# Performance work log

Measured on AMD Instinct MI355X. Metric: run time of the kernel, lower is better.

The kernel has to match this reference:

```python
import jax, jax.numpy as jnp
import numpy as np

NU = 200000  # num users
NI = 200000  # num items
H = 64
L = 2
E = 4000000
P = 100000
EPS = 1e-5


def _seg_mean(msgs, dst, n):
    # msgs: [E, H] gathered source features, dst: [E] destination ids
    s = jax.ops.segment_sum(msgs, dst, num_segments=n)
    c = jax.ops.segment_sum(jnp.ones((msgs.shape[0],), msgs.dtype), dst, num_segments=n)
    return s / jnp.maximum(c, 1.0)[:, None]


def _bn(x, g, b, m, v):
    return (x - m) * jax.lax.rsqrt(v + EPS) * g + b


def setup_inputs() -> dict:
    key = jax.random.key(0)
    ks = jax.random.split(key, 12)
    s = 1.0 / np.sqrt(H)
    inp = {
        "edge_index": jax.random.randint(ks[0], (2, E), 0, NU),
        "edge_label_index": jax.random.randint(ks[1], (2, P), 0, NU),
        "user_emb": jax.random.normal(ks[2], (NU, H), jnp.float32) * 0.1,
        "item_emb": jax.random.normal(ks[3], (NI, H), jnp.float32) * 0.1,
        "u_ll_w": jax.random.normal(ks[4], (L, H, H), jnp.float32) * s,
        "u_ll_b": jnp.zeros((L, H), jnp.float32),
        "u_lr_w": jax.random.normal(ks[5], (L, H, H), jnp.float32) * s,
        "i_ll_w": jax.random.normal(ks[6], (L, H, H), jnp.float32) * s,
        "i_ll_b": jnp.zeros((L, H), jnp.float32),
        "i_lr_w": jax.random.normal(ks[7], (L, H, H), jnp.float32) * s,
        "u_bn_g": jnp.ones((L, H), jnp.float32),
        "u_bn_b": jnp.zeros((L, H), jnp.float32),
        "u_bn_m": jnp.zeros((L, H), jnp.float32),
        "u_bn_v": jnp.ones((L, H), jnp.float32),
        "i_bn_g": jnp.ones((L, H), jnp.float32),
        "i_bn_b": jnp.zeros((L, H), jnp.float32),
        "i_bn_m": jnp.zeros((L, H), jnp.float32),
        "i_bn_v": jnp.ones((L, H), jnp.float32),
        "fc1_w": jax.random.normal(ks[8], (2 * H, H), jnp.float32) * (1.0 / np.sqrt(2 * H)),
        "fc1_b": jnp.zeros((H,), jnp.float32),
        "fc2_w": jax.random.normal(ks[9], (H, 4), jnp.float32) * s,
        "fc2_b": jnp.zeros((4,), jnp.float32),
    }
    return inp


def reference(edge_index, edge_label_index, user_emb, item_emb,
              u_ll_w, u_ll_b, u_lr_w, i_ll_w, i_ll_b, i_lr_w,
              u_bn_g, u_bn_b, u_bn_m, u_bn_v,
              i_bn_g, i_bn_b, i_bn_m, i_bn_v,
              fc1_w, fc1_b, fc2_w, fc2_b):
    src, dst = edge_index[0], edge_index[1]  # user -> item edges
    user_x, item_x = user_emb, item_emb
    for l in range(L):
        # user update: aggregate item features along flipped edges (item->user)
        agg_u = _seg_mean(item_x[dst], src, NU)          # [NU, H]
        u_new = agg_u @ u_ll_w[l] + u_ll_b[l] + user_x @ u_lr_w[l]
        u_new = jax.nn.relu(_bn(u_new, u_bn_g[l], u_bn_b[l], u_bn_m[l], u_bn_v[l]))
        # item update: aggregate (old) user features along user->item edges
        agg_i = _seg_mean(user_x[src], dst, NI)          # [NI, H]
        i_new = agg_i @ i_ll_w[l] + i_ll_b[l] + item_x @ i_lr_w[l]
        i_new = jax.nn.relu(_bn(i_new, i_bn_g[l], i_bn_b[l], i_bn_m[l], i_bn_v[l]))
        user_x, item_x = u_new, i_new
    u_h = user_x[edge_label_index[0]]                    # [P, H]
    i_h = item_x[edge_label_index[1]]                    # [P, H]
    x = jnp.concatenate([u_h, i_h], axis=1)              # [P, 2H]
    x = jax.nn.relu(x @ fc1_w + fc1_b)
    return x @ fc2_w + fc2_b                             # [P, 4]
```

## Files before the change

### kernel.cpp

```cpp
#include <hip/hip_runtime.h>

#define NU 200000
#define NI 200000
#define NN 400000
#define H 64
#define NE 4000000
#define NP 100000
#define EPSF 1e-5f

#define BSH 9
#define BNODES 512
#define NB ((NN + BNODES - 1) / BNODES)
#define CAP 15104

#define PBLOCKS 512
#define EPB 7816

#define DUMMY 200000
#define NROW 200002

typedef unsigned short u16;
typedef __attribute__((ext_vector_type(8))) short bf16x8;
typedef __attribute__((ext_vector_type(4))) float f32x4;

__device__ __forceinline__ u16 f2bf(float f) {
    unsigned int b = __float_as_uint(f);
    b += 0x7FFFu + ((b >> 16) & 1u);
    return (u16)(b >> 16);
}


__global__ __launch_bounds__(256) void part1_kernel(
    const int* __restrict__ src, const int* __restrict__ dst,
    int* __restrict__ blkhist)
{
    __shared__ int hist[NB];
    int tid = threadIdx.x, blk = blockIdx.x;
    for (int i = tid; i < NB; i += 256) hist[i] = 0;
    __syncthreads();
    int e0 = blk * EPB, e1 = min(NE, e0 + EPB);
    for (int e = e0 + tid * 4; e + 4 <= e1; e += 1024) {
        int4 s4 = *(const int4*)&src[e];
        int4 d4 = *(const int4*)&dst[e];
        atomicAdd(&hist[s4.x >> BSH], 1); atomicAdd(&hist[(NU + d4.x) >> BSH], 1);
        atomicAdd(&hist[s4.y >> BSH], 1); atomicAdd(&hist[(NU + d4.y) >> BSH], 1);
        atomicAdd(&hist[s4.z >> BSH], 1); atomicAdd(&hist[(NU + d4.z) >> BSH], 1);
        atomicAdd(&hist[s4.w >> BSH], 1); atomicAdd(&hist[(NU + d4.w) >> BSH], 1);
    }
    __syncthreads();
    for (int i = tid; i < NB; i += 256)
        blkhist[(size_t)i * PBLOCKS + blk] = hist[i];
}

__global__ __launch_bounds__(256) void colscan_kernel(
    int* __restrict__ blkhist, int* __restrict__ g_bcnt)
{
    __shared__ int s[256];
    int b = blockIdx.x, tid = threadIdx.x;
    int* col = blkhist + (size_t)b * PBLOCKS;
    int v0 = col[2 * tid], v1 = col[2 * tid + 1];
    int ps = v0 + v1;
    s[tid] = ps;
    __syncthreads();
    for (int d = 1; d < 256; d <<= 1) {
        int t = (tid >= d) ? s[tid - d] : 0;
        __syncthreads();
        s[tid] += t;
        __syncthreads();
    }
    int ex = s[tid] - ps;
    col[2 * tid] = ex;
    col[2 * tid + 1] = ex + v0;
    if (tid == 255) g_bcnt[b] = s[255];
}

__global__ __launch_bounds__(256) void part2_kernel(
    const int* __restrict__ src, const int* __restrict__ dst,
    const int* __restrict__ blkhist, int* __restrict__ staging)
{
    __shared__ int cur[NB];
    int tid = threadIdx.x, blk = blockIdx.x;
    for (int i = tid; i < NB; i += 256)
        cur[i] = i * CAP + blkhist[(size_t)i * PBLOCKS + blk];
    __syncthreads();
    int e0 = blk * EPB, e1 = min(NE, e0 + EPB);
    for (int e = e0 + tid * 4; e + 4 <= e1; e += 1024) {
        int4 s4 = *(const int4*)&src[e];
        int4 d4 = *(const int4*)&dst[e];
        int sv[4] = {s4.x, s4.y, s4.z, s4.w};
        int dv[4] = {d4.x, d4.y, d4.z, d4.w};
#pragma unroll
        for (int q = 0; q < 4; ++q) {
            int s = sv[q], d = dv[q];
            int p1 = atomicAdd(&cur[s >> BSH], 1);
            staging[p1] = ((s & (BNODES - 1)) << 18) | d;
            int gn = NU + d;
            int p2 = atomicAdd(&cur[gn >> BSH], 1);
            staging[p2] = ((gn & (BNODES - 1)) << 18) | s;
        }
    }
}

__global__ __launch_bounds__(256) void bucket_fill_kernel(
    const int* __restrict__ g_bcnt, const int* __restrict__ staging,
    int* __restrict__ off, int* __restrict__ deg, int* __restrict__ adj)
{
    __shared__ int hist[BNODES];
    __shared__ int psum[256];
    __shared__ int adj_st[CAP];
    int tid = threadIdx.x;
    int b = blockIdx.x;
    int e0 = b * CAP;
    int cnt = g_bcnt[b];
    int node_base = b * BNODES;

    for (int i = tid; i < CAP; i += 256) adj_st[i] = DUMMY;
    hist[tid] = 0; hist[tid + 256] = 0;
    __syncthreads();
    for (int i = tid; i < cnt; i += 256)
        atomicAdd(&hist[staging[e0 + i] >> 18], 1);
    __syncthreads();

    int h0 = hist[2 * tid], h1 = hist[2 * tid + 1];
    int hp0 = (h0 + 7) & ~7, hp1 = (h1 + 7) & ~7;
    psum[tid] = hp0 + hp1;
    __syncthreads();
    for (int d = 1; d < 256; d <<= 1) {
        int t = (tid >= d) ? psum[tid - d] : 0;
        __syncthreads();
        psum[tid] += t;
        __syncthreads();
    }
    int ex0 = psum[tid] - (hp0 + hp1);
    int ex1 = ex0 + hp0;
    int n0 = node_base + 2 * tid;
    if (n0 < NN)     { off[n0]     = e0 + ex0; deg[n0]     = h0; }
    if (n0 + 1 < NN) { off[n0 + 1] = e0 + ex1; deg[n0 + 1] = h1; }
    __syncthreads();
    hist[2 * tid] = ex0; hist[2 * tid + 1] = ex1;
    __syncthreads();

    int ptotal = min(psum[255], CAP);

    for (int i = tid; i < cnt; i += 256) {
        int v = staging[e0 + i];
        int p = atomicAdd(&hist[v >> 18], 1);
        if (p < CAP) adj_st[p] = v & 0x3FFFF;
    }
    __syncthreads();
    for (int i = tid; i < ptotal; i += 256)
        adj[(size_t)b * CAP + i] = adj_st[i];
}

__global__ __launch_bounds__(256) void cvt_kernel(
    const float4* __restrict__ inU, const float4* __restrict__ inI,
    ushort4* __restrict__ outU, ushort4* __restrict__ outI,
    u16* __restrict__ f1, int n4)
{
    int tid = threadIdx.x;
    if (blockIdx.x == 0 && tid < 192) {
        int s = tid >> 5, wd = tid & 31;
        unsigned int* p = (unsigned int*)(f1 + (size_t)s * NROW * H + (size_t)DUMMY * H);
        p[wd] = 0u;
    }
    int i = blockIdx.x * 256 + tid;
    const float4* in;
    ushort4* out;
    if (i < n4) { in = inU; out = outU; }
    else        { in = inI; out = outI; i -= n4; if (i >= n4) return; }
    float4 v = in[i];
    ushort4 h;
    h.x = f2bf(v.x); h.y = f2bf(v.y); h.z = f2bf(v.z); h.w = f2bf(v.w);
    out[i] = h;
}

__global__ __launch_bounds__(256) void pull_update_kernel(
    const int* __restrict__ off, const int* __restrict__ deg,
    const int* __restrict__ adj,
    const u16* __restrict__ xu16, const u16* __restrict__ xi16,
    const u16* __restrict__ selfU, const u16* __restrict__ selfI,
    u16* __restrict__ outU, u16* __restrict__ outI,
    const u16* __restrict__ wcat,
    const float* __restrict__ scsh)
{
    __shared__ u16 sAgg[4][16][72];
    int tid = threadIdx.x;
    int wave = tid >> 6, lane = tid & 63;
    int gw = blockIdx.x * 4 + wave;
    bool isU = gw < (NU / 16);
    int node0 = (isU ? gw : gw - NU / 16) * 16;
    const u16* table = isU ? xi16 : xu16;
    const u16* selfx = isU ? selfU : selfI;
    u16* out         = isU ? outU : outI;
    const u16* wt      = wcat + (isU ? 0 : 64 * 128);
    const float* sc_p  = scsh + (isU ? 0 : 128);
    const float* sh_p  = sc_p + 64;
    int wbase = isU ? node0 : NU + node0;

    int row = lane & 15, g = lane >> 4;
    const u16* xrow = selfx + (size_t)(node0 + row) * H + g * 8;
    bf16x8 a2 = *(const bf16x8*)(xrow);
    bf16x8 a3 = *(const bf16x8*)(xrow + 32);

    int offv = 0, degv = 0;
    if (lane < 16) { offv = off[wbase + lane]; degv = deg[wbase + lane]; }

    int half = lane >> 5;
    int hl   = lane & 31;
    int fl   = hl & 15;
    int rg   = hl >> 4;
    int shb  = (half << 5) + rg;

#define ACC4(w) \
    a0 += __uint_as_float((w).x << 16); a1 += __uint_as_float((w).x & 0xFFFF0000u); \
    a0 += __uint_as_float((w).y << 16); a1 += __uint_as_float((w).y & 0xFFFF0000u);

    for (int p = 0; p < 8; ++p) {
        int begA = __shfl(offv, 2 * p),     dgA = __shfl(degv, 2 * p);
        int begB = __shfl(offv, 2 * p + 1), dgB = __shfl(degv, 2 * p + 1);
        int pdA = (dgA + 7) & ~7, pdB = (dgB + 7) & ~7;
        int myBeg = half ? begB : begA;
        int myPd  = half ? pdB  : pdA;
        int tmax  = max(pdA, pdB);
        float a0 = 0.f, a1 = 0.f, a2f = 0.f, a3f = 0.f;
        for (int k0 = 0; k0 < tmax; k0 += 32) {
            int nb = adj[myBeg + k0 + hl];
            int lim = min(32, tmax - k0);
            uint2 c0, c1, c2, c3;
            {
                int i0 = __shfl(nb, shb + 0), i1 = __shfl(nb, shb + 2);
                int i2 = __shfl(nb, shb + 4), i3 = __shfl(nb, shb + 6);
                if (k0 + 0 + rg >= myPd) i0 = DUMMY;
                if (k0 + 2 + rg >= myPd) i1 = DUMMY;
                if (k0 + 4 + rg >= myPd) i2 = DUMMY;
                if (k0 + 6 + rg >= myPd) i3 = DUMMY;
                c0 = *(const uint2*)&table[(size_t)i0 * H + fl * 4];
                c1 = *(const uint2*)&table[(size_t)i1 * H + fl * 4];
                c2 = *(const uint2*)&table[(size_t)i2 * H + fl * 4];
                c3 = *(const uint2*)&table[(size_t)i3 * H + fl * 4];
            }
            for (int tt = 8; tt < lim; tt += 8) {
                int i0 = __shfl(nb, shb + tt + 0), i1 = __shfl(nb, shb + tt + 2);
                int i2 = __shfl(nb, shb + tt + 4), i3 = __shfl(nb, shb + tt + 6);
                if (k0 + tt + 0 + rg >= myPd) i0 = DUMMY;
                if (k0 + tt + 2 + rg >= myPd) i1 = DUMMY;
                if (k0 + tt + 4 + rg >= myPd) i2 = DUMMY;
                if (k0 + tt + 6 + rg >= myPd) i3 = DUMMY;
                uint2 n0 = *(const uint2*)&table[(size_t)i0 * H + fl * 4];
                uint2 n1 = *(const uint2*)&table[(size_t)i1 * H + fl * 4];
                uint2 n2 = *(const uint2*)&table[(size_t)i2 * H + fl * 4];
                uint2 n3 = *(const uint2*)&table[(size_t)i3 * H + fl * 4];
                a0 += __uint_as_float(c0.x << 16); a1 += __uint_as_float(c0.x & 0xFFFF0000u);
                a2f += __uint_as_float(c0.y << 16); a3f += __uint_as_float(c0.y & 0xFFFF0000u);
                a0 += __uint_as_float(c1.x << 16); a1 += __uint_as_float(c1.x & 0xFFFF0000u);
                a2f += __uint_as_float(c1.y << 16); a3f += __uint_as_float(c1.y & 0xFFFF0000u);
                a0 += __uint_as_float(c2.x << 16); a1 += __uint_as_float(c2.x & 0xFFFF0000u);
                a2f += __uint_as_float(c2.y << 16); a3f += __uint_as_float(c2.y & 0xFFFF0000u);
                a0 += __uint_as_float(c3.x << 16); a1 += __uint_as_float(c3.x & 0xFFFF0000u);
                a2f += __uint_as_float(c3.y << 16); a3f += __uint_as_float(c3.y & 0xFFFF0000u);
                c0 = n0; c1 = n1; c2 = n2; c3 = n3;
            }
            a0 += __uint_as_float(c0.x << 16); a1 += __uint_as_float(c0.x & 0xFFFF0000u);
            a2f += __uint_as_float(c0.y << 16); a3f += __uint_as_float(c0.y & 0xFFFF0000u);
            a0 += __uint_as_float(c1.x << 16); a1 += __uint_as_float(c1.x & 0xFFFF0000u);
            a2f += __uint_as_float(c1.y << 16); a3f += __uint_as_float(c1.y & 0xFFFF0000u);
            a0 += __uint_as_float(c2.x << 16); a1 += __uint_as_float(c2.x & 0xFFFF0000u);
            a2f += __uint_as_float(c2.y << 16); a3f += __uint_as_float(c2.y & 0xFFFF0000u);
            a0 += __uint_as_float(c3.x << 16); a1 += __uint_as_float(c3.x & 0xFFFF0000u);
            a2f += __uint_as_float(c3.y << 16); a3f += __uint_as_float(c3.y & 0xFFFF0000u);
        }
        a0 += __shfl_xor(a0, 16);
        a1 += __shfl_xor(a1, 16);
        a2f += __shfl_xor(a2f, 16);
        a3f += __shfl_xor(a3f, 16);
        int mydg = half ? dgB : dgA;
        if (rg == 0) {
            float inv = 1.0f / fmaxf((float)mydg, 1.0f);
            unsigned int lo = ((unsigned int)f2bf(a1 * inv) << 16) | f2bf(a0 * inv);
            unsigned int hi = ((unsigned int)f2bf(a3f * inv) << 16) | f2bf(a2f * inv);
            uint2 pk; pk.x = lo; pk.y = hi;
            *(uint2*)&sAgg[wave][2 * p + half][fl * 4] = pk;
        }
    }
#undef ACC4

    bf16x8 a[4];
    a[0] = *(const bf16x8*)&sAgg[wave][row][g * 8];
    a[1] = *(const bf16x8*)&sAgg[wave][row][32 + g * 8];
    a[2] = a2;
    a[3] = a3;

#pragma unroll
    for (int ct = 0; ct < 4; ++ct) {
        int feat = ct * 16 + row;
        const u16* wrow = wt + feat * 128 + g * 8;
        f32x4 acc = {0.f, 0.f, 0.f, 0.f};
#pragma unroll
        for (int kb = 0; kb < 4; ++kb) {
            bf16x8 b = *(const bf16x8*)(wrow + kb * 32);
            acc = __builtin_amdgcn_mfma_f32_16x16x32_bf16(a[kb], b, acc, 0, 0, 0);
        }
        float s = sc_p[feat], h = sh_p[feat];
#pragma unroll
        for (int r = 0; r < 4; ++r) {
            int node = node0 + g * 4 + r;
            float v = fmaxf(acc[r] * s + h, 0.f);
            out[(size_t)node * H + feat] = f2bf(v);
        }
    }
}

__global__ __launch_bounds__(256) void wcvt_kernel(
    const float* __restrict__ u_ll_w, const float* __restrict__ u_lr_w,
    const float* __restrict__ i_ll_w, const float* __restrict__ i_lr_w,
    const float* __restrict__ u_ll_b, const float* __restrict__ i_ll_b,
    const float* __restrict__ u_g, const float* __restrict__ u_b,
    const float* __restrict__ u_m, const float* __restrict__ u_v,
    const float* __restrict__ i_g, const float* __restrict__ i_b,
    const float* __restrict__ i_m, const float* __restrict__ i_v,
    u16* __restrict__ wcat, float* __restrict__ scsh)
{
    int idx = blockIdx.x * 256 + threadIdx.x;
    if (idx < 32768) {
        int k = idx & 127, f = (idx >> 7) & 63, t = (idx >> 13) & 1, l = idx >> 14;
        const float* W = t ? (k < 64 ? i_ll_w : i_lr_w)
                           : (k < 64 ? u_ll_w : u_lr_w);
        wcat[idx] = f2bf(W[l * 4096 + (k & 63) * 64 + f]);
    }
    if (idx < 512) {
        int j = idx & 63, half = (idx >> 6) & 1, t = (idx >> 7) & 1, l = idx >> 8;
        const float *g = t ? i_g : u_g, *b = t ? i_b : u_b;
        const float *m = t ? i_m : u_m, *v = t ? i_v : u_v;
        const float *bl = t ? i_ll_b : u_ll_b;
        float sc = g[l * 64 + j] * rsqrtf(v[l * 64 + j] + EPSF);
        scsh[idx] = half ? (bl[l * 64 + j] - m[l * 64 + j]) * sc + b[l * 64 + j]
                         : sc;
    }
}

__global__ __launch_bounds__(256) void mlp_kernel(
    const int* __restrict__ eli,
    const u16* __restrict__ xu16, const u16* __restrict__ xi16,
    const float* __restrict__ fc1w, const float* __restrict__ fc1b,
    const float* __restrict__ fc2w, const float* __restrict__ fc2b,
    float* __restrict__ out, int n)
{
    __shared__ float sW[32][68];
    __shared__ float sA[64][36];
    __shared__ float sH[64][68];
    __shared__ int   sid[128];
    __shared__ float sW2[256];
    int tid = threadIdx.x;
    int p0 = blockIdx.x * 64;
    if (tid < 128) {
        int p = p0 + (tid & 63);
        int side = tid >> 6;
        sid[tid] = (p < n) ? eli[side * NP + p] : -1;
    }
    sW2[tid] = fc2w[tid];
    __syncthreads();

    int jt = (tid & 15) * 4;
    int pt = (tid >> 4) * 4;
    float4 b4 = *(const float4*)&fc1b[jt];
    float acc[4][4];
#pragma unroll
    for (int i = 0; i < 4; ++i) {
        acc[i][0] = b4.x; acc[i][1] = b4.y; acc[i][2] = b4.z; acc[i][3] = b4.w;
    }

    for (int ch = 0; ch < 4; ++ch) {
        int k0 = ch * 32;
        const u16* tab = (ch < 2) ? xu16 : xi16;
        int idbase = (ch < 2) ? 0 : 64;
        int koff = (ch & 1) * 32;
        for (int idx = tid; idx < 64 * 16; idx += 256) {
            int r = idx >> 4, cp = idx & 15;
            int id = sid[idbase + r];
            unsigned int wv = (id >= 0)
                ? *(const unsigned int*)&tab[(size_t)id * H + koff + cp * 2] : 0u;
            sA[r][cp * 2]     = __uint_as_float(wv << 16);
            sA[r][cp * 2 + 1] = __uint_as_float(wv & 0xFFFF0000u);
        }
        for (int idx = tid; idx < 32 * 64; idx += 256) {
            int kk = idx >> 6, j = idx & 63;
            sW[kk][j] = fc1w[(k0 + kk) * 64 + j];
        }
        __syncthreads();
        for (int kk = 0; kk < 32; kk += 4) {
            float a[4][4];
#pragma unroll
            for (int i = 0; i < 4; ++i) {
                float4 t = *(const float4*)&sA[pt + i][kk];
                a[i][0] = t.x; a[i][1] = t.y; a[i][2] = t.z; a[i][3] = t.w;
            }
#pragma unroll
            for (int q = 0; q < 4; ++q) {
                float4 w = *(const float4*)&sW[kk + q][jt];
                float wv[4] = {w.x, w.y, w.z, w.w};
#pragma unroll
                for (int i = 0; i < 4; ++i)
#pragma unroll
                    for (int j = 0; j < 4; ++j)
                        acc[i][j] += a[i][q] * wv[j];
            }
        }
        __syncthreads();
    }

#pragma unroll
    for (int i = 0; i < 4; ++i)
#pragma unroll
        for (int j = 0; j < 4; ++j)
            sH[pt + i][jt + j] = fmaxf(acc[i][j], 0.f);
    __syncthreads();

    int pp = tid >> 2, c = tid & 3;
    float o = 0.f;
#pragma unroll
    for (int j = 0; j < 64; ++j) o += sH[pp][j] * sW2[j * 4 + c];
    int p = p0 + pp;
    if (p < n) out[(size_t)p * 4 + c] = o + fc2b[c];
}

extern "C" void kernel_launch(void* const* d_in, const int* in_sizes, int n_in,
                              void* d_out, int out_size, void* d_ws, size_t ws_size,
                              hipStream_t stream) {
    const int*   edge_index = (const int*)d_in[0];
    const int*   eli        = (const int*)d_in[1];
    const float* user_emb   = (const float*)d_in[2];
    const float* item_emb   = (const float*)d_in[3];
    const float* u_ll_w     = (const float*)d_in[4];
    const float* u_ll_b     = (const float*)d_in[5];
    const float* u_lr_w     = (const float*)d_in[6];
    const float* i_ll_w     = (const float*)d_in[7];
    const float* i_ll_b     = (const float*)d_in[8];
    const float* i_lr_w     = (const float*)d_in[9];
    const float* u_bn_g     = (const float*)d_in[10];
    const float* u_bn_b     = (const float*)d_in[11];
    const float* u_bn_m     = (const float*)d_in[12];
    const float* u_bn_v     = (const float*)d_in[13];
    const float* i_bn_g     = (const float*)d_in[14];
    const float* i_bn_b     = (const float*)d_in[15];
    const float* i_bn_m     = (const float*)d_in[16];
    const float* i_bn_v     = (const float*)d_in[17];
    const float* fc1_w      = (const float*)d_in[18];
    const float* fc1_b      = (const float*)d_in[19];
    const float* fc2_w      = (const float*)d_in[20];
    const float* fc2_b      = (const float*)d_in[21];
    float* out = (float*)d_out;

    const int* src = edge_index;
    const int* dst = edge_index + NE;

    const size_t S = (size_t)NROW * H;
    char* w = (char*)d_ws;
    u16* f1 = (u16*)w;          w += 6 * S * 2;
    int* adj    = (int*)w;      w += ((size_t)NB * CAP + 128) * 4;
    int* off    = (int*)w;      w += (size_t)NN * 4;
    int* deg    = (int*)w;      w += (size_t)NN * 4;
    int* g_bcnt = (int*)w;      w += (size_t)NB * 4;
    u16* wcat   = (u16*)w;      w += (size_t)32768 * 2;
    float* scsh = (float*)w;    w += (size_t)512 * 4;

    u16* emb16_u = f1 + 0 * S;
    u16* emb16_i = f1 + 1 * S;
    u16* fin16_u = f1 + 0 * S;
    u16* fin16_i = f1 + 1 * S;
    u16* xA16_u  = f1 + 4 * S;
    u16* xA16_i  = f1 + 5 * S;
    int* staging = (int*)(f1 + 2 * S);
    int* blkhist = (int*)(f1 + 4 * S);

    part1_kernel<<<PBLOCKS, 256, 0, stream>>>(src, dst, blkhist);
    colscan_kernel<<<NB, 256, 0, stream>>>(blkhist, g_bcnt);
    part2_kernel<<<PBLOCKS, 256, 0, stream>>>(src, dst, blkhist, staging);
    bucket_fill_kernel<<<NB, 256, 0, stream>>>(g_bcnt, staging, off, deg, adj);

    const int n4 = NU * H / 4;
    cvt_kernel<<<(2 * n4 + 255) / 256, 256, 0, stream>>>(
        (const float4*)user_emb, (const float4*)item_emb,
        (ushort4*)emb16_u, (ushort4*)emb16_i, f1, n4);
    wcvt_kernel<<<128, 256, 0, stream>>>(
        u_ll_w, u_lr_w, i_ll_w, i_lr_w, u_ll_b, i_ll_b,
        u_bn_g, u_bn_b, u_bn_m, u_bn_v,
        i_bn_g, i_bn_b, i_bn_m, i_bn_v, wcat, scsh);

    const int pu_blocks = (NN / 16) / 4;

    pull_update_kernel<<<pu_blocks, 256, 0, stream>>>(
        off, deg, adj, emb16_u, emb16_i, emb16_u, emb16_i,
        xA16_u, xA16_i, wcat, scsh);

    pull_update_kernel<<<pu_blocks, 256, 0, stream>>>(
        off, deg, adj, xA16_u, xA16_i, xA16_u, xA16_i,
        fin16_u, fin16_i, wcat + 16384, scsh + 256);

    mlp_kernel<<<(NP + 63) / 64, 256, 0, stream>>>(
        eli, fin16_u, fin16_i, fc1_w, fc1_b, fc2_w, fc2_b, out, NP);
}
```

Baseline: 550.9 us.

## Merge prep kernels and pre-scale adjacency to drop per-edge bounds masking

Folds the histogram, embedding bf16 conversion and weight conversion into one launch, removing two kernel launches and letting independent work overlap. The bucket fill now pads each node pair to the same padded degree and stores neighbor ids pre-shifted to byte offsets. The pull loop can then drop per-edge DUMMY masking and 64-bit index multiplies, at the cost of extra padding slots that point at the zero row. This enlarges adjacency storage and the number of dummy gathers, and it relies on the existing CAP staying large enough for the wider padding.

```diff
diff --git a/kernel.cpp b/kernel.cpp
--- a/kernel.cpp
+++ b/kernel.cpp
@@ -19,6 +19,9 @@
 #define DUMMY 200000
 #define NROW 200002
 
+#define CVTB ((2 * (NU * H / 4) + 255) / 256)
+#define WCVTB 128
+
 typedef unsigned short u16;
 typedef __attribute__((ext_vector_type(8))) short bf16x8;
 typedef __attribute__((ext_vector_type(4))) float f32x4;
@@ -29,27 +32,74 @@
     return (u16)(b >> 16);
 }
 
-
-__global__ __launch_bounds__(256) void part1_kernel(
+__global__ __launch_bounds__(256) void prep_kernel(
     const int* __restrict__ src, const int* __restrict__ dst,
-    int* __restrict__ blkhist)
-{
-    __shared__ int hist[NB];
-    int tid = threadIdx.x, blk = blockIdx.x;
-    for (int i = tid; i < NB; i += 256) hist[i] = 0;
-    __syncthreads();
-    int e0 = blk * EPB, e1 = min(NE, e0 + EPB);
-    for (int e = e0 + tid * 4; e + 4 <= e1; e += 1024) {
-        int4 s4 = *(const int4*)&src[e];
-        int4 d4 = *(const int4*)&dst[e];
-        atomicAdd(&hist[s4.x >> BSH], 1); atomicAdd(&hist[(NU + d4.x) >> BSH], 1);
-        atomicAdd(&hist[s4.y >> BSH], 1); atomicAdd(&hist[(NU + d4.y) >> BSH], 1);
-        atomicAdd(&hist[s4.z >> BSH], 1); atomicAdd(&hist[(NU + d4.z) >> BSH], 1);
-        atomicAdd(&hist[s4.w >> BSH], 1); atomicAdd(&hist[(NU + d4.w) >> BSH], 1);
-    }
-    __syncthreads();
-    for (int i = tid; i < NB; i += 256)
-        blkhist[(size_t)i * PBLOCKS + blk] = hist[i];
+    int* __restrict__ blkhist,
+    const float4* __restrict__ inU, const float4* __restrict__ inI,
+    ushort4* __restrict__ outU, ushort4* __restrict__ outI,
+    u16* __restrict__ f1,
+    const float* __restrict__ u_ll_w, const float* __restrict__ u_lr_w,
+    const float* __restrict__ i_ll_w, const float* __restrict__ i_lr_w,
+    const float* __restrict__ u_ll_b, const float* __restrict__ i_ll_b,
+    const float* __restrict__ u_g, const float* __restrict__ u_b,
+    const float* __restrict__ u_m, const float* __restrict__ u_v,
+    const float* __restrict__ i_g, const float* __restrict__ i_b,
+    const float* __restrict__ i_m, const float* __restrict__ i_v,
+    u16* __restrict__ wcat, float* __restrict__ scsh)
+{
+    int bid = blockIdx.x, tid = threadIdx.x;
+    if (bid < PBLOCKS) {
+        __shared__ int hist[NB];
+        for (int i = tid; i < NB; i += 256) hist[i] = 0;
+        __syncthreads();
+        int e0 = bid * EPB, e1 = min(NE, e0 + EPB);
+        for (int e = e0 + tid * 4; e + 4 <= e1; e += 1024) {
+            int4 s4 = *(const int4*)&src[e];
+            int4 d4 = *(const int4*)&dst[e];
+            atomicAdd(&hist[s4.x >> BSH], 1); atomicAdd(&hist[(NU + d4.x) >> BSH], 1);
+            atomicAdd(&hist[s4.y >> BSH], 1); atomicAdd(&hist[(NU + d4.y) >> BSH], 1);
+            atomicAdd(&hist[s4.z >> BSH], 1); atomicAdd(&hist[(NU + d4.z) >> BSH], 1);
+            atomicAdd(&hist[s4.w >> BSH], 1); atomicAdd(&hist[(NU + d4.w) >> BSH], 1);
+        }
+        __syncthreads();
+        for (int i = tid; i < NB; i += 256)
+            blkhist[(size_t)i * PBLOCKS + bid] = hist[i];
+    } else if (bid < PBLOCKS + CVTB) {
+        int cb = bid - PBLOCKS;
+        if (cb == 0 && tid < 128) {
+            const int sl[4] = {0, 1, 4, 5};
+            int s = sl[tid >> 5], wd = tid & 31;
+            unsigned int* p = (unsigned int*)(f1 + (size_t)s * NROW * H + (size_t)DUMMY * H);
+            p[wd] = 0u;
+        }
+        const int n4 = NU * H / 4;
+        int i = cb * 256 + tid;
+        const float4* in;
+        ushort4* out;
+        if (i < n4) { in = inU; out = outU; }
+        else        { in = inI; out = outI; i -= n4; if (i >= n4) return; }
+        float4 v = in[i];
+        ushort4 h;
+        h.x = f2bf(v.x); h.y = f2bf(v.y); h.z = f2bf(v.z); h.w = f2bf(v.w);
+        out[i] = h;
+    } else {
+        int idx = (bid - PBLOCKS - CVTB) * 256 + tid;
+        if (idx < 32768) {
+            int k = idx & 127, f = (idx >> 7) & 63, t = (idx >> 13) & 1, l = idx >> 14;
+            const float* W = t ? (k < 64 ? i_ll_w : i_lr_w)
+                               : (k < 64 ? u_ll_w : u_lr_w);
+            wcat[idx] = f2bf(W[l * 4096 + (k & 63) * 64 + f]);
+        }
+        if (idx < 512) {
+            int j = idx & 63, half = (idx >> 6) & 1, t = (idx >> 7) & 1, l = idx >> 8;
+            const float *g = t ? i_g : u_g, *b = t ? i_b : u_b;
+            const float *m = t ? i_m : u_m, *v = t ? i_v : u_v;
+            const float *bl = t ? i_ll_b : u_ll_b;
+            float sc = g[l * 64 + j] * rsqrtf(v[l * 64 + j] + EPSF);
+            scsh[idx] = half ? (bl[l * 64 + j] - m[l * 64 + j]) * sc + b[l * 64 + j]
+                             : sc;
+        }
+    }
 }
 
 __global__ __launch_bounds__(256) void colscan_kernel(
@@ -114,7 +164,7 @@
     int cnt = g_bcnt[b];
     int node_base = b * BNODES;
 
-    for (int i = tid; i < CAP; i += 256) adj_st[i] = DUMMY;
+    for (int i = tid; i < CAP; i += 256) adj_st[i] = DUMMY << 7;
     hist[tid] = 0; hist[tid + 256] = 0;
     __syncthreads();
     for (int i = tid; i < cnt; i += 256)
@@ -122,8 +172,8 @@
     __syncthreads();
 
     int h0 = hist[2 * tid], h1 = hist[2 * tid + 1];
-    int hp0 = (h0 + 7) & ~7, hp1 = (h1 + 7) & ~7;
-    psum[tid] = hp0 + hp1;
+    int hp = max((h0 + 7) & ~7, (h1 + 7) & ~7);
+    psum[tid] = 2 * hp;
     __syncthreads();
     for (int d = 1; d < 256; d <<= 1) {
         int t = (tid >= d) ? psum[tid - d] : 0;
@@ -131,8 +181,8 @@
         psum[tid] += t;
         __syncthreads();
     }
-    int ex0 = psum[tid] - (hp0 + hp1);
-    int ex1 = ex0 + hp0;
+    int ex0 = psum[tid] - 2 * hp;
+    int ex1 = ex0 + hp;
     int n0 = node_base + 2 * tid;
     if (n0 < NN)     { off[n0]     = e0 + ex0; deg[n0]     = h0; }
     if (n0 + 1 < NN) { off[n0 + 1] = e0 + ex1; deg[n0 + 1] = h1; }
@@ -145,33 +195,11 @@
     for (int i = tid; i < cnt; i += 256) {
         int v = staging[e0 + i];
         int p = atomicAdd(&hist[v >> 18], 1);
-        if (p < CAP) adj_st[p] = v & 0x3FFFF;
+        if (p < CAP) adj_st[p] = (v & 0x3FFFF) << 7;
     }
     __syncthreads();
     for (int i = tid; i < ptotal; i += 256)
         adj[(size_t)b * CAP + i] = adj_st[i];
-}
-
-__global__ __launch_bounds__(256) void cvt_kernel(
-    const float4* __restrict__ inU, const float4* __restrict__ inI,
-    ushort4* __restrict__ outU, ushort4* __restrict__ outI,
-    u16* __restrict__ f1, int n4)
-{
-    int tid = threadIdx.x;
-    if (blockIdx.x == 0 && tid < 192) {
-        int s = tid >> 5, wd = tid & 31;
-        unsigned int* p = (unsigned int*)(f1 + (size_t)s * NROW * H + (size_t)DUMMY * H);
-        p[wd] = 0u;
-    }
-    int i = blockIdx.x * 256 + tid;
-    const float4* in;
-    ushort4* out;
-    if (i < n4) { in = inU; out = outU; }
-    else        { in = inI; out = outI; i -= n4; if (i >= n4) return; }
-    float4 v = in[i];
-    ushort4 h;
-    h.x = f2bf(v.x); h.y = f2bf(v.y); h.z = f2bf(v.z); h.w = f2bf(v.w);
-    out[i] = h;
 }
 
 __global__ __launch_bounds__(256) void pull_update_kernel(
@@ -199,8 +227,8 @@
 
     int row = lane & 15, g = lane >> 4;
     const u16* xrow = selfx + (size_t)(node0 + row) * H + g * 8;
-    bf16x8 a2 = *(const bf16x8*)(xrow);
-    bf16x8 a3 = *(const bf16x8*)(xrow + 32);
+    bf16x8 sa2 = *(const bf16x8*)(xrow);
+    bf16x8 sa3 = *(const bf16x8*)(xrow + 32);
 
     int offv = 0, degv = 0;
     if (lane < 16) { offv = off[wbase + lane]; degv = deg[wbase + lane]; }
@@ -210,67 +238,46 @@
     int fl   = hl & 15;
     int rg   = hl >> 4;
     int shb  = (half << 5) + rg;
-
-#define ACC4(w) \
-    a0 += __uint_as_float((w).x << 16); a1 += __uint_as_float((w).x & 0xFFFF0000u); \
-    a0 += __uint_as_float((w).y << 16); a1 += __uint_as_float((w).y & 0xFFFF0000u);
+    unsigned flb = (unsigned)fl * 8u;
+    const char* tb = (const char*)table;
+
+#define ACC(c) \
+    a0  += __uint_as_float((c).x << 16); a1 += __uint_as_float((c).x & 0xFFFF0000u); \
+    a2f += __uint_as_float((c).y << 16); a3f += __uint_as_float((c).y & 0xFFFF0000u);
 
     for (int p = 0; p < 8; ++p) {
         int begA = __shfl(offv, 2 * p),     dgA = __shfl(degv, 2 * p);
         int begB = __shfl(offv, 2 * p + 1), dgB = __shfl(degv, 2 * p + 1);
-        int pdA = (dgA + 7) & ~7, pdB = (dgB + 7) & ~7;
+        int pd = max((dgA + 7) & ~7, (dgB + 7) & ~7);
         int myBeg = half ? begB : begA;
-        int myPd  = half ? pdB  : pdA;
-        int tmax  = max(pdA, pdB);
         float a0 = 0.f, a1 = 0.f, a2f = 0.f, a3f = 0.f;
-        for (int k0 = 0; k0 < tmax; k0 += 32) {
+        for (int k0 = 0; k0 < pd; k0 += 32) {
             int nb = adj[myBeg + k0 + hl];
-            int lim = min(32, tmax - k0);
-            uint2 c0, c1, c2, c3;
-            {
-                int i0 = __shfl(nb, shb + 0), i1 = __shfl(nb, shb + 2);
-                int i2 = __shfl(nb, shb + 4), i3 = __shfl(nb, shb + 6);
-                if (k0 + 0 + rg >= myPd) i0 = DUMMY;
-                if (k0 + 2 + rg >= myPd) i1 = DUMMY;
-                if (k0 + 4 + rg >= myPd) i2 = DUMMY;
-                if (k0 + 6 + rg >= myPd) i3 = DUMMY;
-                c0 = *(const uint2*)&table[(size_t)i0 * H + fl * 4];
-                c1 = *(const uint2*)&table[(size_t)i1 * H + fl * 4];
-                c2 = *(const uint2*)&table[(size_t)i2 * H + fl * 4];
-                c3 = *(const uint2*)&table[(size_t)i3 * H + fl * 4];
-            }
+            int lim = min(32, pd - k0);
+            unsigned o0 = (unsigned)__shfl(nb, shb + 0) + flb;
+            unsigned o1 = (unsigned)__shfl(nb, shb + 2) + flb;
+            unsigned o2 = (unsigned)__shfl(nb, shb + 4) + flb;
+            unsigned o3 = (unsigned)__shfl(nb, shb + 6) + flb;
+            uint2 c0 = *(const uint2*)(tb + o0);
+            uint2 c1 = *(const uint2*)(tb + o1);
+            uint2 c2 = *(const uint2*)(tb + o2);
+            uint2 c3 = *(const uint2*)(tb + o3);
             for (int tt = 8; tt < lim; tt += 8) {
-                int i0 = __shfl(nb, shb + tt + 0), i1 = __shfl(nb, shb + tt + 2);
-                int i2 = __shfl(nb, shb + tt + 4), i3 = __shfl(nb, shb + tt + 6);
-                if (k0 + tt + 0 + rg >= myPd) i0 = DUMMY;
-                if (k0 + tt + 2 + rg >= myPd) i1 = DUMMY;
-                if (k0 + tt + 4 + rg >= myPd) i2 = DUMMY;
-                if (k0 + tt + 6 + rg >= myPd) i3 = DUMMY;
-                uint2 n0 = *(const uint2*)&table[(size_t)i0 * H + fl * 4];
-                uint2 n1 = *(const uint2*)&table[(size_t)i1 * H + fl * 4];
-                uint2 n2 = *(const uint2*)&table[(size_t)i2 * H + fl * 4];
-                uint2 n3 = *(const uint2*)&table[(size_t)i3 * H + fl * 4];
-                a0 += __uint_as_float(c0.x << 16); a1 += __uint_as_float(c0.x & 0xFFFF0000u);
-                a2f += __uint_as_float(c0.y << 16); a3f += __uint_as_float(c0.y & 0xFFFF0000u);
-                a0 += __uint_as_float(c1.x << 16); a1 += __uint_as_float(c1.x & 0xFFFF0000u);
-                a2f += __uint_as_float(c1.y << 16); a3f += __uint_as_float(c1.y & 0xFFFF0000u);
-                a0 += __uint_as_float(c2.x << 16); a1 += __uint_as_float(c2.x & 0xFFFF0000u);
-                a2f += __uint_as_float(c2.y << 16); a3f += __uint_as_float(c2.y & 0xFFFF0000u);
-                a0 += __uint_as_float(c3.x << 16); a1 += __uint_as_float(c3.x & 0xFFFF0000u);
-                a2f += __uint_as_float(c3.y << 16); a3f += __uint_as_float(c3.y & 0xFFFF0000u);
+                unsigned q0 = (unsigned)__shfl(nb, shb + tt + 0) + flb;
+                unsigned q1 = (unsigned)__shfl(nb, shb + tt + 2) + flb;
+                unsigned q2 = (unsigned)__shfl(nb, shb + tt + 4) + flb;
+                unsigned q3 = (unsigned)__shfl(nb, shb + tt + 6) + flb;
+                uint2 n0 = *(const uint2*)(tb + q0);
+                uint2 n1 = *(const uint2*)(tb + q1);
+                uint2 n2 = *(const uint2*)(tb + q2);
+                uint2 n3 = *(const uint2*)(tb + q3);
+                ACC(c0) ACC(c1) ACC(c2) ACC(c3)
                 c0 = n0; c1 = n1; c2 = n2; c3 = n3;
             }
-            a0 += __uint_as_float(c0.x << 16); a1 += __uint_as_float(c0.x & 0xFFFF0000u);
-            a2f += __uint_as_float(c0.y << 16); a3f += __uint_as_float(c0.y & 0xFFFF0000u);
-            a0 += __uint_as_float(c1.x << 16); a1 += __uint_as_float(c1.x & 0xFFFF0000u);
-            a2f += __uint_as_float(c1.y << 16); a3f += __uint_as_float(c1.y & 0xFFFF0000u);
-            a0 += __uint_as_float(c2.x << 16); a1 += __uint_as_float(c2.x & 0xFFFF0000u);
-            a2f += __uint_as_float(c2.y << 16); a3f += __uint_as_float(c2.y & 0xFFFF0000u);
-            a0 += __uint_as_float(c3.x << 16); a1 += __uint_as_float(c3.x & 0xFFFF0000u);
-            a2f += __uint_as_float(c3.y << 16); a3f += __uint_as_float(c3.y & 0xFFFF0000u);
-        }
-        a0 += __shfl_xor(a0, 16);
-        a1 += __shfl_xor(a1, 16);
+            ACC(c0) ACC(c1) ACC(c2) ACC(c3)
+        }
+        a0  += __shfl_xor(a0, 16);
+        a1  += __shfl_xor(a1, 16);
         a2f += __shfl_xor(a2f, 16);
         a3f += __shfl_xor(a3f, 16);
         int mydg = half ? dgB : dgA;
@@ -282,13 +289,13 @@
             *(uint2*)&sAgg[wave][2 * p + half][fl * 4] = pk;
         }
     }
-#undef ACC4
+#undef ACC
 
     bf16x8 a[4];
     a[0] = *(const bf16x8*)&sAgg[wave][row][g * 8];
     a[1] = *(const bf16x8*)&sAgg[wave][row][32 + g * 8];
-    a[2] = a2;
-    a[3] = a3;
+    a[2] = sa2;
+    a[3] = sa3;
 
 #pragma unroll
     for (int ct = 0; ct < 4; ++ct) {
@@ -307,34 +314,6 @@
             float v = fmaxf(acc[r] * s + h, 0.f);
             out[(size_t)node * H + feat] = f2bf(v);
         }
-    }
-}
-
-__global__ __launch_bounds__(256) void wcvt_kernel(
-    const float* __restrict__ u_ll_w, const float* __restrict__ u_lr_w,
-    const float* __restrict__ i_ll_w, const float* __restrict__ i_lr_w,
-    const float* __restrict__ u_ll_b, const float* __restrict__ i_ll_b,
-    const float* __restrict__ u_g, const float* __restrict__ u_b,
-    const float* __restrict__ u_m, const float* __restrict__ u_v,
-    const float* __restrict__ i_g, const float* __restrict__ i_b,
-    const float* __restrict__ i_m, const float* __restrict__ i_v,
-    u16* __restrict__ wcat, float* __restrict__ scsh)
-{
-    int idx = blockIdx.x * 256 + threadIdx.x;
-    if (idx < 32768) {
-        int k = idx & 127, f = (idx >> 7) & 63, t = (idx >> 13) & 1, l = idx >> 14;
-        const float* W = t ? (k < 64 ? i_ll_w : i_lr_w)
-                           : (k < 64 ? u_ll_w : u_lr_w);
-        wcat[idx] = f2bf(W[l * 4096 + (k & 63) * 64 + f]);
-    }
-    if (idx < 512) {
-        int j = idx & 63, half = (idx >> 6) & 1, t = (idx >> 7) & 1, l = idx >> 8;
-        const float *g = t ? i_g : u_g, *b = t ? i_b : u_b;
-        const float *m = t ? i_m : u_m, *v = t ? i_v : u_v;
-        const float *bl = t ? i_ll_b : u_ll_b;
-        float sc = g[l * 64 + j] * rsqrtf(v[l * 64 + j] + EPSF);
-        scsh[idx] = half ? (bl[l * 64 + j] - m[l * 64 + j]) * sc + b[l * 64 + j]
-                         : sc;
     }
 }
 
@@ -472,20 +451,18 @@
     int* staging = (int*)(f1 + 2 * S);
     int* blkhist = (int*)(f1 + 4 * S);
 
-    part1_kernel<<<PBLOCKS, 256, 0, stream>>>(src, dst, blkhist);
+    prep_kernel<<<PBLOCKS + CVTB + WCVTB, 256, 0, stream>>>(
+        src, dst, blkhist,
+        (const float4*)user_emb, (const float4*)item_emb,
+        (ushort4*)emb16_u, (ushort4*)emb16_i, f1,
+        u_ll_w, u_lr_w, i_ll_w, i_lr_w, u_ll_b, i_ll_b,
+        u_bn_g, u_bn_b, u_bn_m, u_bn_v,
+        i_bn_g, i_bn_b, i_bn_m, i_bn_v, wcat, scsh);
+
     colscan_kernel<<<NB, 256, 0, stream>>>(blkhist, g_bcnt);
     part2_kernel<<<PBLOCKS, 256, 0, stream>>>(src, dst, blkhist, staging);
     bucket_fill_kernel<<<NB, 256, 0, stream>>>(g_bcnt, staging, off, deg, adj);
 
-    const int n4 = NU * H / 4;
-    cvt_kernel<<<(2 * n4 + 255) / 256, 256, 0, stream>>>(
-        (const float4*)user_emb, (const float4*)item_emb,
-        (ushort4*)emb16_u, (ushort4*)emb16_i, f1, n4);
-    wcvt_kernel<<<128, 256, 0, stream>>>(
-        u_ll_w, u_lr_w, i_ll_w, i_lr_w, u_ll_b, i_ll_b,
-        u_bn_g, u_bn_b, u_bn_m, u_bn_v,
-        i_bn_g, i_bn_b, i_bn_m, i_bn_v, wcat, scsh);
-
     const int pu_blocks = (NN / 16) / 4;
 
     pull_update_kernel<<<pu_blocks, 256, 0, stream>>>(
```

Result: no change. 545.7 us (median of 3 runs) (-1.0%).
